# Kernel tuning notes

Hardware: AMD Instinct MI355X
Metric: run time of the kernel (lower is better)

Reference implementation:

```python
import jax, jax.numpy as jnp
import numpy as np

SHIFT_MIN, SHIFT_MAX = -14.0, 0.0  # deepshift range for weight_bits=5: (-(2**4-2), 0)


def shift_quant(w):
    """Quantize weights to signed powers of two (bit-shift weights), STE form."""
    sign = jnp.sign(w)
    shift = jnp.clip(jnp.round(jnp.log2(jnp.abs(w) + 1e-12)), SHIFT_MIN, SHIFT_MAX)
    q = sign * jnp.exp2(shift)
    return w + jax.lax.stop_gradient(q - w)


def moe_fc(t, wg, w0, b0, w1, b1):
    """Top-1 routing over 2 experts: expert0 dense Linear, expert1 shift-quantized Linear.
    t: [T, C]; weights torch-layout [out, in]. With top_k=1 the softmaxed top-k gate is 1.0,
    so combine is a hard select of the chosen expert's output."""
    logits = t @ wg                      # [T, 2]
    pick0 = (jnp.argmax(logits, axis=-1) == 0)[:, None]
    y0 = t @ w0.T + b0                   # dense expert
    y1 = t @ shift_quant(w1).T + b1      # shift expert
    return jnp.where(pick0, y0, y1)


def setup_inputs() -> dict:
    key = jax.random.key(0)
    ks = jax.random.split(key, 10)
    B, N, C, Dh = 16, 1024, 512, 2048
    s = 0.02
    return {
        "x": jax.random.normal(ks[0], (B, N, C), jnp.float32),
        "H": 32,
        "W": 32,
        "wg1": jax.random.normal(ks[1], (C, 2), jnp.float32) * s,
        "fc1_w0": jax.random.normal(ks[2], (Dh, C), jnp.float32) * s,
        "fc1_b0": jnp.zeros((Dh,), jnp.float32),
        "fc1_w1": jax.random.normal(ks[3], (Dh, C), jnp.float32) * s,
        "fc1_b1": jnp.zeros((Dh,), jnp.float32),
        "dw_w": jax.random.normal(ks[4], (Dh, 1, 3, 3), jnp.float32) * np.sqrt(2.0 / 9.0),
        "dw_b": jnp.zeros((Dh,), jnp.float32),
        "wg2": jax.random.normal(ks[5], (Dh, 2), jnp.float32) * s,
        "fc2_w0": jax.random.normal(ks[6], (C, Dh), jnp.float32) * s,
        "fc2_b0": jnp.zeros((C,), jnp.float32),
        "fc2_w1": jax.random.normal(ks[7], (C, Dh), jnp.float32) * s,
        "fc2_b1": jnp.zeros((C,), jnp.float32),
    }


def reference(x, H, W, wg1, fc1_w0, fc1_b0, fc1_w1, fc1_b1, dw_w, dw_b,
              wg2, fc2_w0, fc2_b0, fc2_w1, fc2_b1):
    B, N, C = x.shape
    Dh = fc1_w0.shape[0]
    # fc1 MoE
    h = moe_fc(x.reshape(-1, C), wg1, fc1_w0, fc1_b0, fc1_w1, fc1_b1)  # [B*N, Dh]
    # DWConv 3x3 depthwise, NCHW
    h = h.reshape(B, N, Dh).transpose(0, 2, 1).reshape(B, Dh, H, W)
    h = jax.lax.conv_general_dilated(
        h, dw_w, window_strides=(1, 1), padding="SAME",
        dimension_numbers=("NCHW", "OIHW", "NCHW"), feature_group_count=Dh)
    h = h + dw_b[None, :, None, None]
    h = h.reshape(B, Dh, N).transpose(0, 2, 1)  # [B, N, Dh]
    # GELU (exact, as nn.GELU default); dropout p=0 -> identity
    h = jax.nn.gelu(h, approximate=False)
    # fc2 MoE
    y = moe_fc(h.reshape(-1, Dh), wg2, fc2_w0, fc2_b0, fc2_w1, fc2_b1)
    return y.reshape(B, N, -1)
```

## Files before the change

kernel.cpp:

```cpp
#include <hip/hip_runtime.h>
#include <hip/hip_bf16.h>


#define TOKS  16384
#define CIN   512
#define DHID  2048

typedef __attribute__((ext_vector_type(8))) __bf16 bf16x8;
typedef __attribute__((ext_vector_type(4))) float  f32x4;
typedef __attribute__((ext_vector_type(4))) float  float4v;
typedef __attribute__((ext_vector_type(4))) unsigned short ushort4v;

__device__ __forceinline__ unsigned short f2bf(float f) {
  union { float f; unsigned int u; } a; a.f = f;
  unsigned int u = a.u;
  unsigned int r = u + 0x7FFFu + ((u >> 16) & 1u);
  return (unsigned short)(r >> 16);
}
__device__ __forceinline__ float bf2f(unsigned short h) {
  union { unsigned int u; float f; } a; a.u = ((unsigned int)h) << 16;
  return a.f;
}

__device__ __forceinline__ float squant(float w) {
  float aw = fabsf(w) + 1e-12f;
  double l = log2((double)aw);
  double r = rint(l);
  r = fmin(fmax(r, -14.0), 0.0);
  float q = exp2f((float)r);
  return (w > 0.0f) ? q : ((w < 0.0f) ? -q : 0.0f);
}

#define GLDS16(gp, lp) __builtin_amdgcn_global_load_lds(                      \
    (const __attribute__((address_space(1))) void*)(gp),                      \
    (__attribute__((address_space(3))) void*)(lp), 16, 0, 0)

__global__ void k_prep(const float* __restrict__ w0, const float* __restrict__ w1,
                       const float* __restrict__ w20, const float* __restrict__ w21,
                       unsigned short* __restrict__ w0hi, unsigned short* __restrict__ w0lo,
                       unsigned short* __restrict__ w1q, unsigned short* __restrict__ w20b,
                       unsigned short* __restrict__ w21b) {
  int i = blockIdx.x * 256 + threadIdx.x;
  if (i >= DHID * CIN) return;
  float v = w0[i];
  unsigned short h = f2bf(v);
  w0hi[i] = h;
  w0lo[i] = f2bf(v - bf2f(h));
  w1q[i]  = f2bf(squant(w1[i]));
  w20b[i] = f2bf(w20[i]);
  w21b[i] = f2bf(squant(w21[i]));
}

__global__ void k_gate1(const float* __restrict__ x, const float* __restrict__ wg1,
                        unsigned char* __restrict__ pick1) {
  int tok = blockIdx.x * 4 + (threadIdx.x >> 6);
  int l = threadIdx.x & 63;
  const float* xr = x + (size_t)tok * CIN;
  float s0 = 0.f, s1 = 0.f;
  for (int i = l; i < CIN; i += 64) {
    float v = xr[i];
    s0 += v * wg1[i * 2 + 0];
    s1 += v * wg1[i * 2 + 1];
  }
  for (int m = 32; m; m >>= 1) { s0 += __shfl_xor(s0, m); s1 += __shfl_xor(s1, m); }
  if (l == 0) pick1[tok] = (s0 >= s1) ? 0 : 1;
}

__launch_bounds__(256, 2)
__global__ void k_fc1(const float* __restrict__ x,
                      const unsigned short* __restrict__ w0hi,
                      const unsigned short* __restrict__ w0lo,
                      const unsigned short* __restrict__ w1q,
                      const float* __restrict__ b0, const float* __restrict__ b1,
                      const unsigned char* __restrict__ pick1,
                      float* __restrict__ h32) {
  __shared__ unsigned short lAh[128][40];
  __shared__ unsigned short lAl[128][40];
  __shared__ unsigned short lB0h[128][32];
  __shared__ unsigned short lB0l[128][32];
  __shared__ unsigned short lB1q[128][32];

  const int t = threadIdx.x;
  const int wv = t >> 6, ln = t & 63;
  const int lr = ln & 15, lg = ln >> 4;
  const int tok0 = blockIdx.x * 128;
  const int nbase = blockIdx.y * 128;
  const int wm = (wv >> 1) * 64, wn = (wv & 1) * 64;

  f32x4 acc0[4][4], acc1[4][4];
  #pragma unroll
  for (int i = 0; i < 4; ++i)
    #pragma unroll
    for (int j = 0; j < 4; ++j) {
      acc0[i][j] = f32x4{0.f, 0.f, 0.f, 0.f};
      acc1[i][j] = f32x4{0.f, 0.f, 0.f, 0.f};
    }

  for (int kt = 0; kt < CIN / 32; ++kt) {
    const int k0 = kt * 32;
    float4v av[4];
    #pragma unroll
    for (int p = 0; p < 4; ++p) {
      int idx = p * 256 + t;
      int row = idx >> 3;
      int c4 = (idx & 7) << 2;
      av[p] = *(const float4v*)(x + (size_t)(tok0 + row) * CIN + k0 + c4);
    }
    __syncthreads();
    #pragma unroll
    for (int s = 0; s < 2; ++s) {
      int rowblk = s * 4 + wv;
      int row = (rowblk << 4) + (ln >> 2);
      int cg = (ln & 3) << 3;
      size_t go = (size_t)(nbase + row) * CIN + k0 + cg;
      GLDS16(w0hi + go, &lB0h[rowblk << 4][0]);
      GLDS16(w0lo + go, &lB0l[rowblk << 4][0]);
      GLDS16(w1q + go, &lB1q[rowblk << 4][0]);
    }
    #pragma unroll
    for (int p = 0; p < 4; ++p) {
      int idx = p * 256 + t;
      int row = idx >> 3;
      int c4 = (idx & 7) << 2;
      ushort4v hv, lv;
      #pragma unroll
      for (int q = 0; q < 4; ++q) {
        float v = av[p][q];
        unsigned short h = f2bf(v);
        hv[q] = h;
        lv[q] = f2bf(v - bf2f(h));
      }
      *(ushort4v*)(&lAh[row][c4]) = hv;
      *(ushort4v*)(&lAl[row][c4]) = lv;
    }
    __syncthreads();

    bf16x8 ah[4], al[4];
    #pragma unroll
    for (int mt = 0; mt < 4; ++mt) {
      ah[mt] = *(const bf16x8*)(&lAh[wm + (mt << 4) + lr][lg << 3]);
      al[mt] = *(const bf16x8*)(&lAl[wm + (mt << 4) + lr][lg << 3]);
    }
    #pragma unroll
    for (int nt = 0; nt < 4; ++nt) {
      bf16x8 bh = *(const bf16x8*)(&lB0h[wn + (nt << 4) + lr][lg << 3]);
      bf16x8 bl = *(const bf16x8*)(&lB0l[wn + (nt << 4) + lr][lg << 3]);
      bf16x8 bq = *(const bf16x8*)(&lB1q[wn + (nt << 4) + lr][lg << 3]);
      #pragma unroll
      for (int mt = 0; mt < 4; ++mt) {
        acc0[mt][nt] = __builtin_amdgcn_mfma_f32_16x16x32_bf16(ah[mt], bh, acc0[mt][nt], 0, 0, 0);
        acc0[mt][nt] = __builtin_amdgcn_mfma_f32_16x16x32_bf16(al[mt], bh, acc0[mt][nt], 0, 0, 0);
        acc0[mt][nt] = __builtin_amdgcn_mfma_f32_16x16x32_bf16(ah[mt], bl, acc0[mt][nt], 0, 0, 0);
        acc1[mt][nt] = __builtin_amdgcn_mfma_f32_16x16x32_bf16(ah[mt], bq, acc1[mt][nt], 0, 0, 0);
        acc1[mt][nt] = __builtin_amdgcn_mfma_f32_16x16x32_bf16(al[mt], bq, acc1[mt][nt], 0, 0, 0);
      }
    }
  }
  #pragma unroll
  for (int nt = 0; nt < 4; ++nt) {
    int d = nbase + wn + (nt << 4) + lr;
    float bi0 = b0[d], bi1 = b1[d];
    #pragma unroll
    for (int mt = 0; mt < 4; ++mt) {
      f32x4 v0 = acc0[mt][nt], v1 = acc1[mt][nt];
      #pragma unroll
      for (int rr = 0; rr < 4; ++rr) {
        int tok = tok0 + wm + (mt << 4) + (lg << 2) + rr;
        float val = pick1[tok] ? (v1[rr] + bi1) : (v0[rr] + bi0);
        h32[(size_t)tok * DHID + d] = val;
      }
    }
  }
}

__global__ void k_conv(const float* __restrict__ h32, const float* __restrict__ dww,
                       const float* __restrict__ dwb, const float* __restrict__ wg2,
                       unsigned short* __restrict__ hb, float* __restrict__ part) {
  __shared__ float tile[10][32][32];
  const int dc = blockIdx.x;
  const int ys = blockIdx.y;
  const int b  = blockIdx.z;
  const int t = threadIdx.x;
  const int d0 = dc * 32, y0 = ys * 8;

  for (int p = 0; p < 10240; p += 256) {
    int idx = p + t;
    int dl = idx & 31, xx = (idx >> 5) & 31, ry = idx >> 10;
    int y = y0 - 1 + ry;
    float v = 0.f;
    if (y >= 0 && y < 32)
      v = h32[(size_t)(b * 1024 + y * 32 + xx) * DHID + d0 + dl];
    tile[ry][xx][dl] = v;
  }
  __syncthreads();

  const int dl = t & 31, xg = t >> 5;
  const int d = d0 + dl;
  float kk[9];
  #pragma unroll
  for (int i = 0; i < 9; ++i) kk[i] = dww[d * 9 + i];
  const float bias = dwb[d];
  const float g0 = wg2[d * 2 + 0], g1 = wg2[d * 2 + 1];

  for (int yy = 0; yy < 8; ++yy) {
    int ry = yy + 1;
    #pragma unroll
    for (int xi = 0; xi < 4; ++xi) {
      int xx = xg * 4 + xi;
      float s = bias;
      #pragma unroll
      for (int dy = -1; dy <= 1; ++dy)
        #pragma unroll
        for (int dx = -1; dx <= 1; ++dx) {
          int xs = xx + dx;
          float v = (xs >= 0 && xs < 32) ? tile[ry + dy][xs][dl] : 0.f;
          s += v * kk[(dy + 1) * 3 + (dx + 1)];
        }
      float gg = 0.5f * s * (1.0f + erff(s * 0.70710678118654752f));
      int tok = b * 1024 + (y0 + yy) * 32 + xx;
      hb[(size_t)tok * DHID + d] = f2bf(gg);
      float p0 = gg * g0, p1 = gg * g1;
      for (int m = 16; m; m >>= 1) { p0 += __shfl_xor(p0, m); p1 += __shfl_xor(p1, m); }
      if (dl == 0) {
        part[(size_t)tok * 128 + 0 * 64 + dc] = p0;
        part[(size_t)tok * 128 + 1 * 64 + dc] = p1;
      }
    }
  }
}

__global__ void k_gate2(const float* __restrict__ part, unsigned char* __restrict__ pick2) {
  int tok = blockIdx.x * 256 + threadIdx.x;
  const float* pr = part + (size_t)tok * 128;
  float s0 = 0.f, s1 = 0.f;
  for (int i = 0; i < 64; ++i) { s0 += pr[i]; s1 += pr[64 + i]; }
  pick2[tok] = (s0 >= s1) ? 0 : 1;
}

__launch_bounds__(256, 2)
__global__ void k_fc2(const unsigned short* __restrict__ hb,
                      const unsigned short* __restrict__ w20b,
                      const unsigned short* __restrict__ w21b,
                      const float* __restrict__ b0, const float* __restrict__ b1,
                      const unsigned char* __restrict__ pick2,
                      float* __restrict__ out) {
  __shared__ unsigned short lA[128][32];
  __shared__ unsigned short lB0[128][32];
  __shared__ unsigned short lB1[128][32];
  const int t = threadIdx.x;
  const int wv = t >> 6, ln = t & 63;
  const int lr = ln & 15, lg = ln >> 4;
  const int tok0 = blockIdx.x * 128;
  const int nbase = blockIdx.y * 128;
  const int wm = (wv >> 1) * 64, wn = (wv & 1) * 64;

  f32x4 acc0[4][4], acc1[4][4];
  #pragma unroll
  for (int i = 0; i < 4; ++i)
    #pragma unroll
    for (int j = 0; j < 4; ++j) {
      acc0[i][j] = f32x4{0.f, 0.f, 0.f, 0.f};
      acc1[i][j] = f32x4{0.f, 0.f, 0.f, 0.f};
    }

  for (int kt = 0; kt < DHID / 32; ++kt) {
    const int k0 = kt * 32;
    __syncthreads();
    #pragma unroll
    for (int s = 0; s < 2; ++s) {
      int rowblk = s * 4 + wv;
      int row = (rowblk << 4) + (ln >> 2);
      int cg = (ln & 3) << 3;
      size_t goA = (size_t)(tok0 + row) * DHID + k0 + cg;
      size_t goB = (size_t)(nbase + row) * DHID + k0 + cg;
      GLDS16(hb + goA, &lA[rowblk << 4][0]);
      GLDS16(w20b + goB, &lB0[rowblk << 4][0]);
      GLDS16(w21b + goB, &lB1[rowblk << 4][0]);
    }
    __syncthreads();
    bf16x8 a[4];
    #pragma unroll
    for (int mt = 0; mt < 4; ++mt)
      a[mt] = *(const bf16x8*)(&lA[wm + (mt << 4) + lr][lg << 3]);
    #pragma unroll
    for (int nt = 0; nt < 4; ++nt) {
      bf16x8 b0f = *(const bf16x8*)(&lB0[wn + (nt << 4) + lr][lg << 3]);
      bf16x8 b1f = *(const bf16x8*)(&lB1[wn + (nt << 4) + lr][lg << 3]);
      #pragma unroll
      for (int mt = 0; mt < 4; ++mt) {
        acc0[mt][nt] = __builtin_amdgcn_mfma_f32_16x16x32_bf16(a[mt], b0f, acc0[mt][nt], 0, 0, 0);
        acc1[mt][nt] = __builtin_amdgcn_mfma_f32_16x16x32_bf16(a[mt], b1f, acc1[mt][nt], 0, 0, 0);
      }
    }
  }
  #pragma unroll
  for (int nt = 0; nt < 4; ++nt) {
    int c = nbase + wn + (nt << 4) + lr;
    float bi0 = b0[c], bi1 = b1[c];
    #pragma unroll
    for (int mt = 0; mt < 4; ++mt) {
      f32x4 v0 = acc0[mt][nt], v1 = acc1[mt][nt];
      #pragma unroll
      for (int rr = 0; rr < 4; ++rr) {
        int tok = tok0 + wm + (mt << 4) + (lg << 2) + rr;
        float val = pick2[tok] ? (v1[rr] + bi1) : (v0[rr] + bi0);
        out[(size_t)tok * CIN + c] = val;
      }
    }
  }
}

extern "C" void kernel_launch(void* const* d_in, const int* in_sizes, int n_in,
                              void* d_out, int out_size, void* d_ws, size_t ws_size,
                              hipStream_t stream) {
  (void)in_sizes; (void)n_in; (void)out_size; (void)ws_size;
  const float* x   = (const float*)d_in[0];
  const float* wg1 = (const float*)d_in[3];
  const float* w0  = (const float*)d_in[4];
  const float* b0  = (const float*)d_in[5];
  const float* w1  = (const float*)d_in[6];
  const float* b1  = (const float*)d_in[7];
  const float* dww = (const float*)d_in[8];
  const float* dwb = (const float*)d_in[9];
  const float* wg2 = (const float*)d_in[10];
  const float* w20 = (const float*)d_in[11];
  const float* b20 = (const float*)d_in[12];
  const float* w21 = (const float*)d_in[13];
  const float* b21 = (const float*)d_in[14];
  float* out = (float*)d_out;

  char* ws = (char*)d_ws;
  const size_t MB2 = 1u << 21;
  unsigned short* w0hi = (unsigned short*)(ws + 0 * MB2);
  unsigned short* w0lo = (unsigned short*)(ws + 1 * MB2);
  unsigned short* w1q  = (unsigned short*)(ws + 2 * MB2);
  unsigned short* w20b = (unsigned short*)(ws + 3 * MB2);
  unsigned short* w21b = (unsigned short*)(ws + 4 * MB2);
  unsigned char* pick1 = (unsigned char*)(ws + 5 * MB2);
  unsigned char* pick2 = (unsigned char*)(ws + 5 * MB2 + 65536);
  float* part = (float*)(ws + 5 * MB2 + 131072);
  float* h32  = (float*)(ws + 5 * MB2 + 131072 + (size_t)TOKS * 128 * 4);
  unsigned short* hb = (unsigned short*)((char*)h32 + (size_t)TOKS * DHID * 4);

  k_prep <<<4096, 256, 0, stream>>>(w0, w1, w20, w21, w0hi, w0lo, w1q, w20b, w21b);
  k_gate1<<<4096, 256, 0, stream>>>(x, wg1, pick1);
  k_fc1  <<<dim3(128, 16), 256, 0, stream>>>(x, w0hi, w0lo, w1q, b0, b1, pick1, h32);
  k_conv <<<dim3(64, 4, 16), 256, 0, stream>>>(h32, dww, dwb, wg2, hb, part);
  k_gate2<<<64, 256, 0, stream>>>(part, pick2);
  k_fc2  <<<dim3(128, 4), 256, 0, stream>>>(hb, w20b, w21b, b20, b21, pick2, out);
}
```

Baseline: 389.8 us.

## Sort tokens by expert and compute only the chosen expert per tile

Adds a single-block scan kernel that builds a permutation grouping tokens by their gate choice, then fc1 and fc2 gather rows through that permutation and skip the unused expert's weight loads and MFMAs for tiles that are entirely one expert. Before this, both experts were computed for every token and then selected. The change also swizzles the LDS B/A layout to reduce bank conflicts, replaces the double-precision log2 in shift quantization with exponent bit arithmetic, and parallelizes the gate2 reduction across a wavefront. Costs are two extra serial scan launches, gathered row loads and scattered output stores.

```diff
diff --git a/kernel.cpp b/kernel.cpp
--- a/kernel.cpp
+++ b/kernel.cpp
@@ -23,12 +23,15 @@
 }
 
 __device__ __forceinline__ float squant(float w) {
+  if (w == 0.0f) return 0.0f;
   float aw = fabsf(w) + 1e-12f;
-  double l = log2((double)aw);
-  double r = rint(l);
-  r = fmin(fmax(r, -14.0), 0.0);
-  float q = exp2f((float)r);
-  return (w > 0.0f) ? q : ((w < 0.0f) ? -q : 0.0f);
+  union { float f; unsigned u; } a; a.f = aw;
+  int e = (int)((a.u >> 23) & 0xFFu) - 127;
+  unsigned frac = a.u & 0x7FFFFFu;
+  int shift = e + (frac >= 0x3504F4u ? 1 : 0);
+  shift = min(max(shift, -14), 0);
+  union { unsigned u; float f; } q; q.u = (unsigned)(shift + 127) << 23;
+  return (w > 0.0f) ? q.f : -q.f;
 }
 
 #define GLDS16(gp, lp) __builtin_amdgcn_global_load_lds(                      \
@@ -66,13 +69,41 @@
   if (l == 0) pick1[tok] = (s0 >= s1) ? 0 : 1;
 }
 
+__global__ void k_scan(const unsigned char* __restrict__ pick, int* __restrict__ perm,
+                       int* __restrict__ n0buf) {
+  __shared__ int cnt[1024];
+  const int t = threadIdx.x;
+  unsigned char loc[16];
+  int c0 = 0;
+  #pragma unroll
+  for (int i = 0; i < 16; ++i) { loc[i] = pick[t * 16 + i]; c0 += (loc[i] == 0); }
+  cnt[t] = c0;
+  __syncthreads();
+  for (int off = 1; off < 1024; off <<= 1) {
+    int v = cnt[t] + ((t >= off) ? cnt[t - off] : 0);
+    __syncthreads();
+    cnt[t] = v;
+    __syncthreads();
+  }
+  int total0 = cnt[1023];
+  int pre0 = cnt[t] - c0;
+  int pre1 = t * 16 - pre0;
+  if (t == 0) n0buf[0] = total0;
+  int p0 = pre0, p1 = total0 + pre1;
+  #pragma unroll
+  for (int i = 0; i < 16; ++i) {
+    int tok = t * 16 + i;
+    if (loc[i] == 0) perm[p0++] = tok; else perm[p1++] = tok;
+  }
+}
+
 __launch_bounds__(256, 2)
 __global__ void k_fc1(const float* __restrict__ x,
                       const unsigned short* __restrict__ w0hi,
                       const unsigned short* __restrict__ w0lo,
                       const unsigned short* __restrict__ w1q,
                       const float* __restrict__ b0, const float* __restrict__ b1,
-                      const unsigned char* __restrict__ pick1,
+                      const int* __restrict__ perm, const int* __restrict__ n0buf,
                       float* __restrict__ h32) {
   __shared__ unsigned short lAh[128][40];
   __shared__ unsigned short lAl[128][40];
@@ -86,6 +117,16 @@
   const int tok0 = blockIdx.x * 128;
   const int nbase = blockIdx.y * 128;
   const int wm = (wv >> 1) * 64, wn = (wv & 1) * 64;
+  const int n0 = n0buf[0];
+  const bool do0 = (tok0 < n0);
+  const bool do1 = (tok0 + 128 > n0);
+
+  int prow[4];
+  #pragma unroll
+  for (int p = 0; p < 4; ++p) prow[p] = perm[tok0 + ((p * 256 + t) >> 3)];
+
+  const int swsrc = ((ln & 3) ^ ((ln >> 3) & 3)) << 3;
+  const int swrd  = (lg ^ ((lr >> 1) & 3)) << 3;
 
   f32x4 acc0[4][4], acc1[4][4];
   #pragma unroll
@@ -102,26 +143,24 @@
     #pragma unroll
     for (int p = 0; p < 4; ++p) {
       int idx = p * 256 + t;
-      int row = idx >> 3;
-      int c4 = (idx & 7) << 2;
-      av[p] = *(const float4v*)(x + (size_t)(tok0 + row) * CIN + k0 + c4);
+      av[p] = *(const float4v*)(x + (size_t)prow[p] * CIN + k0 + ((idx & 7) << 2));
     }
     __syncthreads();
     #pragma unroll
     for (int s = 0; s < 2; ++s) {
       int rowblk = s * 4 + wv;
       int row = (rowblk << 4) + (ln >> 2);
-      int cg = (ln & 3) << 3;
-      size_t go = (size_t)(nbase + row) * CIN + k0 + cg;
-      GLDS16(w0hi + go, &lB0h[rowblk << 4][0]);
-      GLDS16(w0lo + go, &lB0l[rowblk << 4][0]);
-      GLDS16(w1q + go, &lB1q[rowblk << 4][0]);
+      size_t go = (size_t)(nbase + row) * CIN + k0 + swsrc;
+      if (do0) {
+        GLDS16(w0hi + go, &lB0h[rowblk << 4][0]);
+        GLDS16(w0lo + go, &lB0l[rowblk << 4][0]);
+      }
+      if (do1) GLDS16(w1q + go, &lB1q[rowblk << 4][0]);
     }
     #pragma unroll
     for (int p = 0; p < 4; ++p) {
       int idx = p * 256 + t;
-      int row = idx >> 3;
-      int c4 = (idx & 7) << 2;
+      int row = idx >> 3, c4 = (idx & 7) << 2;
       ushort4v hv, lv;
       #pragma unroll
       for (int q = 0; q < 4; ++q) {
@@ -143,16 +182,24 @@
     }
     #pragma unroll
     for (int nt = 0; nt < 4; ++nt) {
-      bf16x8 bh = *(const bf16x8*)(&lB0h[wn + (nt << 4) + lr][lg << 3]);
-      bf16x8 bl = *(const bf16x8*)(&lB0l[wn + (nt << 4) + lr][lg << 3]);
-      bf16x8 bq = *(const bf16x8*)(&lB1q[wn + (nt << 4) + lr][lg << 3]);
-      #pragma unroll
-      for (int mt = 0; mt < 4; ++mt) {
-        acc0[mt][nt] = __builtin_amdgcn_mfma_f32_16x16x32_bf16(ah[mt], bh, acc0[mt][nt], 0, 0, 0);
-        acc0[mt][nt] = __builtin_amdgcn_mfma_f32_16x16x32_bf16(al[mt], bh, acc0[mt][nt], 0, 0, 0);
-        acc0[mt][nt] = __builtin_amdgcn_mfma_f32_16x16x32_bf16(ah[mt], bl, acc0[mt][nt], 0, 0, 0);
-        acc1[mt][nt] = __builtin_amdgcn_mfma_f32_16x16x32_bf16(ah[mt], bq, acc1[mt][nt], 0, 0, 0);
-        acc1[mt][nt] = __builtin_amdgcn_mfma_f32_16x16x32_bf16(al[mt], bq, acc1[mt][nt], 0, 0, 0);
+      int rB = wn + (nt << 4) + lr;
+      if (do0) {
+        bf16x8 bh = *(const bf16x8*)(&lB0h[rB][swrd]);
+        bf16x8 bl = *(const bf16x8*)(&lB0l[rB][swrd]);
+        #pragma unroll
+        for (int mt = 0; mt < 4; ++mt) {
+          acc0[mt][nt] = __builtin_amdgcn_mfma_f32_16x16x32_bf16(ah[mt], bh, acc0[mt][nt], 0, 0, 0);
+          acc0[mt][nt] = __builtin_amdgcn_mfma_f32_16x16x32_bf16(al[mt], bh, acc0[mt][nt], 0, 0, 0);
+          acc0[mt][nt] = __builtin_amdgcn_mfma_f32_16x16x32_bf16(ah[mt], bl, acc0[mt][nt], 0, 0, 0);
+        }
+      }
+      if (do1) {
+        bf16x8 bq = *(const bf16x8*)(&lB1q[rB][swrd]);
+        #pragma unroll
+        for (int mt = 0; mt < 4; ++mt) {
+          acc1[mt][nt] = __builtin_amdgcn_mfma_f32_16x16x32_bf16(ah[mt], bq, acc1[mt][nt], 0, 0, 0);
+          acc1[mt][nt] = __builtin_amdgcn_mfma_f32_16x16x32_bf16(al[mt], bq, acc1[mt][nt], 0, 0, 0);
+        }
       }
     }
   }
@@ -165,8 +212,9 @@
       f32x4 v0 = acc0[mt][nt], v1 = acc1[mt][nt];
       #pragma unroll
       for (int rr = 0; rr < 4; ++rr) {
-        int tok = tok0 + wm + (mt << 4) + (lg << 2) + rr;
-        float val = pick1[tok] ? (v1[rr] + bi1) : (v0[rr] + bi0);
+        int pos = tok0 + wm + (mt << 4) + (lg << 2) + rr;
+        int tok = perm[pos];
+        float val = (pos >= n0) ? (v1[rr] + bi1) : (v0[rr] + bi0);
         h32[(size_t)tok * DHID + d] = val;
       }
     }
@@ -222,19 +270,20 @@
       float p0 = gg * g0, p1 = gg * g1;
       for (int m = 16; m; m >>= 1) { p0 += __shfl_xor(p0, m); p1 += __shfl_xor(p1, m); }
       if (dl == 0) {
-        part[(size_t)tok * 128 + 0 * 64 + dc] = p0;
-        part[(size_t)tok * 128 + 1 * 64 + dc] = p1;
+        part[(size_t)tok * 128 + dc] = p0;
+        part[(size_t)tok * 128 + 64 + dc] = p1;
       }
     }
   }
 }
 
 __global__ void k_gate2(const float* __restrict__ part, unsigned char* __restrict__ pick2) {
-  int tok = blockIdx.x * 256 + threadIdx.x;
+  int tok = blockIdx.x * 4 + (threadIdx.x >> 6);
+  int l = threadIdx.x & 63;
   const float* pr = part + (size_t)tok * 128;
-  float s0 = 0.f, s1 = 0.f;
-  for (int i = 0; i < 64; ++i) { s0 += pr[i]; s1 += pr[64 + i]; }
-  pick2[tok] = (s0 >= s1) ? 0 : 1;
+  float s0 = pr[l], s1 = pr[64 + l];
+  for (int m = 32; m; m >>= 1) { s0 += __shfl_xor(s0, m); s1 += __shfl_xor(s1, m); }
+  if (l == 0) pick2[tok] = (s0 >= s1) ? 0 : 1;
 }
 
 __launch_bounds__(256, 2)
@@ -242,7 +291,7 @@
                       const unsigned short* __restrict__ w20b,
                       const unsigned short* __restrict__ w21b,
                       const float* __restrict__ b0, const float* __restrict__ b1,
-                      const unsigned char* __restrict__ pick2,
+                      const int* __restrict__ perm, const int* __restrict__ n0buf,
                       float* __restrict__ out) {
   __shared__ unsigned short lA[128][32];
   __shared__ unsigned short lB0[128][32];
@@ -253,6 +302,17 @@
   const int tok0 = blockIdx.x * 128;
   const int nbase = blockIdx.y * 128;
   const int wm = (wv >> 1) * 64, wn = (wv & 1) * 64;
+  const int n0 = n0buf[0];
+  const bool do0 = (tok0 < n0);
+  const bool do1 = (tok0 + 128 > n0);
+
+  const int swsrc = ((ln & 3) ^ ((ln >> 3) & 3)) << 3;
+  const int swrd  = (lg ^ ((lr >> 1) & 3)) << 3;
+
+  int arow[2];
+  #pragma unroll
+  for (int s = 0; s < 2; ++s)
+    arow[s] = perm[tok0 + ((s * 4 + wv) << 4) + (ln >> 2)];
 
   f32x4 acc0[4][4], acc1[4][4];
   #pragma unroll
@@ -270,26 +330,30 @@
     for (int s = 0; s < 2; ++s) {
       int rowblk = s * 4 + wv;
       int row = (rowblk << 4) + (ln >> 2);
-      int cg = (ln & 3) << 3;
-      size_t goA = (size_t)(tok0 + row) * DHID + k0 + cg;
-      size_t goB = (size_t)(nbase + row) * DHID + k0 + cg;
-      GLDS16(hb + goA, &lA[rowblk << 4][0]);
-      GLDS16(w20b + goB, &lB0[rowblk << 4][0]);
-      GLDS16(w21b + goB, &lB1[rowblk << 4][0]);
+      size_t goB = (size_t)(nbase + row) * DHID + k0 + swsrc;
+      GLDS16(hb + (size_t)arow[s] * DHID + k0 + swsrc, &lA[rowblk << 4][0]);
+      if (do0) GLDS16(w20b + goB, &lB0[rowblk << 4][0]);
+      if (do1) GLDS16(w21b + goB, &lB1[rowblk << 4][0]);
     }
     __syncthreads();
     bf16x8 a[4];
     #pragma unroll
     for (int mt = 0; mt < 4; ++mt)
-      a[mt] = *(const bf16x8*)(&lA[wm + (mt << 4) + lr][lg << 3]);
+      a[mt] = *(const bf16x8*)(&lA[wm + (mt << 4) + lr][swrd]);
     #pragma unroll
     for (int nt = 0; nt < 4; ++nt) {
-      bf16x8 b0f = *(const bf16x8*)(&lB0[wn + (nt << 4) + lr][lg << 3]);
-      bf16x8 b1f = *(const bf16x8*)(&lB1[wn + (nt << 4) + lr][lg << 3]);
-      #pragma unroll
-      for (int mt = 0; mt < 4; ++mt) {
-        acc0[mt][nt] = __builtin_amdgcn_mfma_f32_16x16x32_bf16(a[mt], b0f, acc0[mt][nt], 0, 0, 0);
-        acc1[mt][nt] = __builtin_amdgcn_mfma_f32_16x16x32_bf16(a[mt], b1f, acc1[mt][nt], 0, 0, 0);
+      int rB = wn + (nt << 4) + lr;
+      if (do0) {
+        bf16x8 b0f = *(const bf16x8*)(&lB0[rB][swrd]);
+        #pragma unroll
+        for (int mt = 0; mt < 4; ++mt)
+          acc0[mt][nt] = __builtin_amdgcn_mfma_f32_16x16x32_bf16(a[mt], b0f, acc0[mt][nt], 0, 0, 0);
+      }
+      if (do1) {
+        bf16x8 b1f = *(const bf16x8*)(&lB1[rB][swrd]);
+        #pragma unroll
+        for (int mt = 0; mt < 4; ++mt)
+          acc1[mt][nt] = __builtin_amdgcn_mfma_f32_16x16x32_bf16(a[mt], b1f, acc1[mt][nt], 0, 0, 0);
       }
     }
   }
@@ -302,8 +366,9 @@
       f32x4 v0 = acc0[mt][nt], v1 = acc1[mt][nt];
       #pragma unroll
       for (int rr = 0; rr < 4; ++rr) {
-        int tok = tok0 + wm + (mt << 4) + (lg << 2) + rr;
-        float val = pick2[tok] ? (v1[rr] + bi1) : (v0[rr] + bi0);
+        int pos = tok0 + wm + (mt << 4) + (lg << 2) + rr;
+        int tok = perm[pos];
+        float val = (pos >= n0) ? (v1[rr] + bi1) : (v0[rr] + bi0);
         out[(size_t)tok * CIN + c] = val;
       }
     }
@@ -336,16 +401,23 @@
   unsigned short* w1q  = (unsigned short*)(ws + 2 * MB2);
   unsigned short* w20b = (unsigned short*)(ws + 3 * MB2);
   unsigned short* w21b = (unsigned short*)(ws + 4 * MB2);
-  unsigned char* pick1 = (unsigned char*)(ws + 5 * MB2);
-  unsigned char* pick2 = (unsigned char*)(ws + 5 * MB2 + 65536);
-  float* part = (float*)(ws + 5 * MB2 + 131072);
-  float* h32  = (float*)(ws + 5 * MB2 + 131072 + (size_t)TOKS * 128 * 4);
-  unsigned short* hb = (unsigned short*)((char*)h32 + (size_t)TOKS * DHID * 4);
+  char* p = ws + 5 * MB2;
+  unsigned char* pick1 = (unsigned char*)p;            p += 65536;
+  unsigned char* pick2 = (unsigned char*)p;            p += 65536;
+  int* perm1 = (int*)p;                                p += TOKS * 4;
+  int* perm2 = (int*)p;                                p += TOKS * 4;
+  int* n0a   = (int*)p;                                p += 256;
+  int* n0b   = (int*)p;                                p += 256;
+  float* part = (float*)p;                             p += (size_t)TOKS * 128 * 4;
+  float* h32  = (float*)p;                             p += (size_t)TOKS * DHID * 4;
+  unsigned short* hb = (unsigned short*)p;
 
   k_prep <<<4096, 256, 0, stream>>>(w0, w1, w20, w21, w0hi, w0lo, w1q, w20b, w21b);
   k_gate1<<<4096, 256, 0, stream>>>(x, wg1, pick1);
-  k_fc1  <<<dim3(128, 16), 256, 0, stream>>>(x, w0hi, w0lo, w1q, b0, b1, pick1, h32);
+  k_scan <<<1, 1024, 0, stream>>>(pick1, perm1, n0a);
+  k_fc1  <<<dim3(128, 16), 256, 0, stream>>>(x, w0hi, w0lo, w1q, b0, b1, perm1, n0a, h32);
   k_conv <<<dim3(64, 4, 16), 256, 0, stream>>>(h32, dww, dwb, wg2, hb, part);
-  k_gate2<<<64, 256, 0, stream>>>(part, pick2);
-  k_fc2  <<<dim3(128, 4), 256, 0, stream>>>(hb, w20b, w21b, b20, b21, pick2, out);
-}
+  k_gate2<<<4096, 256, 0, stream>>>(part, pick2);
+  k_scan <<<1, 1024, 0, stream>>>(pick2, perm2, n0b);
+  k_fc2  <<<dim3(128, 4), 256, 0, stream>>>(hb, w20b, w21b, b20, b21, perm2, n0b, out);
+}
```

Result: faster. 373.5 us (-4.2%).
